# Kernel optimization log

Hardware: AMD Instinct MI355X
Metric: run time of the kernel (lower is better)

The kernel has to match this reference:

```python
import jax, jax.numpy as jnp
import numpy as np

NF = 64        # num_feat
DG = 16        # deformable_groups
K = 3
KK = K * K
CG = NF // DG  # channels per deformable group


def lrelu(x):
    return jnp.where(x >= 0, x, 0.1 * x)


def conv3x3(x, w, b):
    y = jax.lax.conv_general_dilated(
        x, w, window_strides=(1, 1), padding=((1, 1), (1, 1)),
        dimension_numbers=('NCHW', 'OIHW', 'NCHW'))
    return y + b[None, :, None, None]


def _bilinear(feat, py, px):
    # feat: (C, H, W); py, px: arbitrary shape S -> (C,) + S; zeros outside bounds
    H, W = feat.shape[-2:]
    y0f = jnp.floor(py)
    x0f = jnp.floor(px)
    dy = py - y0f
    dx = px - x0f
    y0 = y0f.astype(jnp.int32)
    x0 = x0f.astype(jnp.int32)
    out = jnp.zeros(feat.shape[:1] + py.shape, feat.dtype)
    for yy, xx, wgt in ((y0, x0, (1 - dy) * (1 - dx)),
                        (y0, x0 + 1, (1 - dy) * dx),
                        (y0 + 1, x0, dy * (1 - dx)),
                        (y0 + 1, x0 + 1, dy * dx)):
        valid = (yy >= 0) & (yy < H) & (xx >= 0) & (xx < W)
        v = feat[:, jnp.clip(yy, 0, H - 1), jnp.clip(xx, 0, W - 1)]
        out = out + v * (wgt * valid)[None]
    return out


def backwarp(x, flow):
    # x: (N,C,H,W); flow: (N,2,H,W) with channels (dx, dy) in pixels
    N, C, H, W = x.shape
    gy, gx = jnp.meshgrid(jnp.arange(H, dtype=x.dtype),
                          jnp.arange(W, dtype=x.dtype), indexing='ij')
    px = gx[None] + flow[:, 0]
    py = gy[None] + flow[:, 1]
    return jax.vmap(_bilinear)(x, py, px)


def dcn_v2(x, offset, mask, w, b):
    # x: (N,C,H,W); offset: (N, DG*KK*2, H, W) as consecutive (dy,dx) pairs;
    # mask: (N, DG*KK, H, W) already sigmoided. stride=1, pad=1, k=3.
    N, C, H, W = x.shape
    off = offset.reshape(N, DG, KK, 2, H, W)
    dy, dx = off[:, :, :, 0], off[:, :, :, 1]            # (N,DG,KK,H,W)
    gy, gx = jnp.meshgrid(jnp.arange(H, dtype=x.dtype),
                          jnp.arange(W, dtype=x.dtype), indexing='ij')
    ky = (jnp.arange(KK) // K - K // 2).astype(x.dtype)  # tap row offset: -1,0,1
    kx = (jnp.arange(KK) % K - K // 2).astype(x.dtype)   # tap col offset
    py = dy + gy[None, None, None] + ky[None, None, :, None, None]
    px = dx + gx[None, None, None] + kx[None, None, :, None, None]
    xg = x.reshape(N, DG, CG, H, W)
    sampled = jax.vmap(jax.vmap(_bilinear))(xg, py, px)  # (N,DG,CG,KK,H,W)
    sampled = sampled * mask.reshape(N, DG, 1, KK, H, W)
    wr = w.reshape(-1, DG, CG, KK)                       # (Cout,DG,CG,KK)
    out = jnp.einsum('ngckhw,ogck->nohw', sampled, wr)
    return out + b[None, :, None, None]


def fgda(nbr_feat, ref_feat, flow, w1, b1, w2, b2, w3, b3, w4, b4, dcn_w, dcn_b):
    warped = backwarp(nbr_feat, flow)
    h = lrelu(conv3x3(jnp.concatenate([warped, ref_feat], axis=1), w1, b1))
    h = lrelu(conv3x3(h, w2, b2))
    h = lrelu(conv3x3(h, w3, b3))
    out = conv3x3(h, w4, b4)                             # (N, DG*27, H, W)
    o1, o2, mask = jnp.split(out, 3, axis=1)
    N, _, H, W = flow.shape
    residual = jnp.concatenate([o1, o2], axis=1).reshape(N, -1, 2, H, W)
    # torch.flip(flow, dims=[1]) -> (flow_y, flow_x), broadcast over all taps
    offset = flow[:, ::-1].reshape(N, 1, 2, H, W) + residual
    offset = offset.reshape(N, -1, H, W)
    mask = jax.nn.sigmoid(mask)
    return lrelu(dcn_v2(nbr_feat, offset, mask, dcn_w, dcn_b))


def setup_inputs():
    key = jax.random.key(0)
    ks = jax.random.split(key, 8)
    N, H, W = 8, 128, 128
    s = 0.05
    return {
        'nbr_feat': jax.random.normal(ks[0], (N, NF, H, W), jnp.float32),
        'ref_feat': jax.random.normal(ks[1], (N, NF, H, W), jnp.float32),
        'flow': jax.random.normal(ks[2], (N, 2, H, W), jnp.float32) * 2.0,
        'w1': jax.random.normal(ks[3], (NF, 2 * NF, 3, 3), jnp.float32) * s,
        'b1': jnp.zeros((NF,), jnp.float32),
        'w2': jax.random.normal(ks[4], (NF, NF, 3, 3), jnp.float32) * s,
        'b2': jnp.zeros((NF,), jnp.float32),
        'w3': jax.random.normal(ks[5], (NF, NF, 3, 3), jnp.float32) * s,
        'b3': jnp.zeros((NF,), jnp.float32),
        'w4': jax.random.normal(ks[6], (DG * 3 * KK, NF, 3, 3), jnp.float32) * s,
        'b4': jnp.zeros((DG * 3 * KK,), jnp.float32),
        'dcn_w': jax.random.normal(ks[7], (NF, NF, 3, 3), jnp.float32) * s,
        'dcn_b': jnp.zeros((NF,), jnp.float32),
    }


def reference(nbr_feat, ref_feat, flow, w1, b1, w2, b2, w3, b3, w4, b4, dcn_w, dcn_b):
    return fgda(nbr_feat, ref_feat, flow, w1, b1, w2, b2, w3, b3, w4, b4, dcn_w, dcn_b)
```

## Files before the change

### kernel.cpp

```cpp
#include <hip/hip_runtime.h>
#include <math.h>

#define H 128
#define W 128
#define NB 8
#define NFC 64

typedef __attribute__((ext_vector_type(8))) short s16x8;
typedef __attribute__((ext_vector_type(4))) short s16x4;
typedef __attribute__((ext_vector_type(4))) float f32x4;
typedef __attribute__((ext_vector_type(4))) int   i32x4;
typedef __attribute__((ext_vector_type(2))) int   i32x2;

__device__ __forceinline__ float b2f(short s) {
    return __uint_as_float(((unsigned)(unsigned short)s) << 16);
}
__device__ __forceinline__ short f2bf(float f) {
    unsigned u = __float_as_uint(f);
    u += 0x7FFF + ((u >> 16) & 1);
    return (short)(u >> 16);
}
__device__ __forceinline__ short f2h(float f) {
    _Float16 h = (_Float16)f;
    return __builtin_bit_cast(short, h);
}
__device__ __forceinline__ float h2f(short s) {
    return (float)__builtin_bit_cast(_Float16, s);
}

__global__ __launch_bounds__(256) void k_wt_all(
    const float* __restrict__ w1, const float* __restrict__ w2,
    const float* __restrict__ w3, const float* __restrict__ w4,
    const float* __restrict__ dcw, short* __restrict__ wp)
{
    int idx = blockIdx.x * 256 + threadIdx.x;
    int u = idx / 576;
    int r = idx - u * 576;
    int t = r >> 6, i = r & 63;
    float v;
    if (u < 128) {
        int o = u & 63, icoff = (u >> 6) << 6;
        v = w1[((size_t)(o * 128) + icoff + i) * 9 + t];
    } else if (u < 192) {
        int o = u - 128;
        v = w2[((size_t)(o * 64) + i) * 9 + t];
    } else if (u < 256) {
        int o = u - 192;
        v = w3[((size_t)(o * 64) + i) * 9 + t];
    } else if (u < 704) {
        int o = u - 256;
        v = (o < 432) ? w4[((size_t)(o * 64) + i) * 9 + t] : 0.f;
    } else {
        int o = u - 704;
        v = dcw[((size_t)(o * 64) + i) * 9 + t];
    }
    wp[idx] = f2bf(v);
}

__global__ __launch_bounds__(256) void k_nhwc2(const float* __restrict__ nbr,
                                               const float* __restrict__ ref,
                                               short* __restrict__ nbrG,
                                               short* __restrict__ refH)
{
    int px = blockIdx.x * 256 + threadIdx.x;
    bool isNbr = (px < 131072);
    const float* src;
    if (isNbr) { src = nbr; }
    else       { src = ref; px -= 131072; }
    int n = px >> 14;
    int sp = px & 16383;
    const float* s = src + (size_t)n * 64 * 16384 + sp;
    unsigned pk[32];
    #pragma unroll
    for (int c = 0; c < 32; ++c) {
        float v0 = s[(size_t)(2 * c) * 16384];
        float v1 = s[(size_t)(2 * c + 1) * 16384];
        pk[c] = (unsigned)(unsigned short)f2bf(v0) |
                ((unsigned)(unsigned short)f2bf(v1) << 16);
    }
    if (isNbr) {
        #pragma unroll
        for (int g = 0; g < 16; ++g) {
            i32x2 t;
            t[0] = pk[2 * g]; t[1] = pk[2 * g + 1];
            *(i32x2*)(nbrG + ((size_t)(n * 16 + g) * 16384 + sp) * 4) = t;
        }
    } else {
        i32x4* d = (i32x4*)(refH + (size_t)(n * 16384 + sp) * 64);
        #pragma unroll
        for (int qq = 0; qq < 8; ++qq) {
            i32x4 t;
            t[0] = pk[4 * qq]; t[1] = pk[4 * qq + 1];
            t[2] = pk[4 * qq + 2]; t[3] = pk[4 * qq + 3];
            d[qq] = t;
        }
    }
}

__global__ __launch_bounds__(256) void k_backwarp(const short* __restrict__ nbrG,
                                                  const float* __restrict__ flow,
                                                  short* __restrict__ warped)
{
    int idx = blockIdx.x * 256 + threadIdx.x;
    int px = idx >> 2, qt = idx & 3;
    int n = px >> 14;
    int x = px & 127, y = (px >> 7) & 127;
    float fx = flow[(size_t)(n * 2 + 0) * 16384 + y * 128 + x];
    float fy = flow[(size_t)(n * 2 + 1) * 16384 + y * 128 + x];
    float pxf = (float)x + fx, pyf = (float)y + fy;
    float x0f = floorf(pxf), y0f = floorf(pyf);
    int x0 = (int)x0f, y0 = (int)y0f;
    float dx = pxf - x0f, dy = pyf - y0f;
    float vy0 = ((unsigned)y0 < 128u) ? 1.f : 0.f;
    float vy1 = ((unsigned)(y0 + 1) < 128u) ? 1.f : 0.f;
    float vx0 = ((unsigned)x0 < 128u) ? 1.f : 0.f;
    float vx1 = ((unsigned)(x0 + 1) < 128u) ? 1.f : 0.f;
    float w00 = (1.f - dy) * (1.f - dx) * vy0 * vx0;
    float w01 = (1.f - dy) * dx * vy0 * vx1;
    float w10 = dy * (1.f - dx) * vy1 * vx0;
    float w11 = dy * dx * vy1 * vx1;
    int y0c = min(max(y0, 0), 127), y1c = min(max(y0 + 1, 0), 127);
    int x0c = min(max(x0, 0), 127), x1c = min(max(x0 + 1, 0), 127);
    int xb = min(max(x0, 0), 126);
    bool s0 = (x0c == xb), s1 = (x1c == xb);

    const short* plbase = nbrG + (size_t)n * 16 * 65536;
    s16x8 r0, r1;
    #pragma unroll
    for (int pg = 0; pg < 4; ++pg) {
        const short* pl = plbase + (size_t)(qt * 4 + pg) * 65536;
        s16x8 p0 = *(const s16x8*)(pl + (y0c * 128 + xb) * 4);
        s16x8 p1 = *(const s16x8*)(pl + (y1c * 128 + xb) * 4);
        #pragma unroll
        for (int cc = 0; cc < 4; ++cc) {
            float v00 = b2f(s0 ? p0[cc] : p0[4 + cc]);
            float v01 = b2f(s1 ? p0[cc] : p0[4 + cc]);
            float v10 = b2f(s0 ? p1[cc] : p1[4 + cc]);
            float v11 = b2f(s1 ? p1[cc] : p1[4 + cc]);
            float v = w00 * v00 + w01 * v01 + w10 * v10 + w11 * v11;
            short res = f2bf(v);
            if (pg < 2) r0[pg * 4 + cc] = res;
            else        r1[(pg - 2) * 4 + cc] = res;
        }
    }
    short* o = warped + (size_t)px * 64 + qt * 16;
    *(s16x8*)o = r0;
    *(s16x8*)(o + 8) = r1;
}

template<int MODE>
__global__ __launch_bounds__(256) void k_conv(
    const short* __restrict__ in, const short* __restrict__ wT,
    const float* __restrict__ bias,
    float* __restrict__ partial, short* __restrict__ outB,
    short* __restrict__ offmask, const float* __restrict__ flow, int n0)
{
    __shared__ __align__(16) short tileS[180 * 64];
    __shared__ __align__(16) short aS[64 * 64];

    int tid = threadIdx.x;
    int bid = blockIdx.x;
    int og = (MODE == 3) ? blockIdx.y : 0;
    int n  = (MODE == 3) ? (n0 + (bid >> 7)) : (bid >> 7);
    int tl = bid & 127;
    int bx = (tl & 7) << 4;
    int by = (tl >> 3) << 3;
    int ln = tid & 63, wv = tid >> 6;
    int c = ln & 15, q = ln >> 4;

    for (int i = tid; i < 1440; i += 256) {
        int pt = i >> 3, c16 = i & 7;
        int ty = pt / 18, tx = pt - ty * 18;
        int gy = by + ty - 1, gx = bx + tx - 1;
        i32x4 v = {0, 0, 0, 0};
        if ((unsigned)gy < 128u && (unsigned)gx < 128u)
            v = *(const i32x4*)(in + (((size_t)n * 128 + gy) * 128 + gx) * 64 + c16 * 8);
        *(i32x4*)((char*)tileS + pt * 128 + ((c16 ^ (pt & 7)) << 4)) = v;
    }

    const short* wbase = wT + ((MODE == 3) ? (size_t)og * 36864 : 0);
    int aoc = tid >> 3, ac8 = tid & 7;
    i32x4 sa0 = *(const i32x4*)(wbase + (size_t)aoc * 576 + ac8 * 8);
    i32x4 sa1 = *(const i32x4*)(wbase + (size_t)(aoc + 32) * 576 + ac8 * 8);

    f32x4 acc[4][2];
    #pragma unroll
    for (int m = 0; m < 4; ++m) {
        acc[m][0] = (f32x4){0.f, 0.f, 0.f, 0.f};
        acc[m][1] = (f32x4){0.f, 0.f, 0.f, 0.f};
    }

    int p0 = 2 * wv, p1 = 2 * wv + 1;
    int pby0 = (p0 >> 2) << 2, pbx0 = (p0 & 3) << 2;
    int pby1 = (p1 >> 2) << 2, pbx1 = (p1 & 3) << 2;
    int cy = c >> 2, cx = c & 3;

    __syncthreads();

    for (int tap = 0; tap < 9; ++tap) {
        *(i32x4*)((char*)aS + aoc * 128 + ((ac8 ^ (aoc & 7)) << 4)) = sa0;
        *(i32x4*)((char*)aS + (aoc + 32) * 128 + ((ac8 ^ ((aoc + 32) & 7)) << 4)) = sa1;
        if (tap < 8) {
            sa0 = *(const i32x4*)(wbase + (size_t)aoc * 576 + (tap + 1) * 64 + ac8 * 8);
            sa1 = *(const i32x4*)(wbase + (size_t)(aoc + 32) * 576 + (tap + 1) * 64 + ac8 * 8);
        }
        __syncthreads();

        int dty = tap / 3, dtx = tap - dty * 3;
        int pta = (pby0 + cy + dty) * 18 + pbx0 + cx + dtx;
        int ptb = (pby1 + cy + dty) * 18 + pbx1 + cx + dtx;
        #pragma unroll
        for (int ih = 0; ih < 2; ++ih) {
            int slot = ih * 4 + q;
            s16x8 bf0 = *(const s16x8*)((const char*)tileS + pta * 128 + ((slot ^ (pta & 7)) << 4));
            s16x8 bf1 = *(const s16x8*)((const char*)tileS + ptb * 128 + ((slot ^ (ptb & 7)) << 4));
            #pragma unroll
            for (int m = 0; m < 4; ++m) {
                int ocl = m * 16 + c;
                s16x8 a = *(const s16x8*)((const char*)aS + ocl * 128 + ((slot ^ (ocl & 7)) << 4));
                acc[m][0] = __builtin_amdgcn_mfma_f32_16x16x32_bf16(a, bf0, acc[m][0], 0, 0, 0);
                acc[m][1] = __builtin_amdgcn_mfma_f32_16x16x32_bf16(a, bf1, acc[m][1], 0, 0, 0);
            }
        }
        __syncthreads();
    }

    #pragma unroll
    for (int p = 0; p < 2; ++p) {
        int pby = p ? pby1 : pby0;
        int pbx = p ? pbx1 : pbx0;
        int y = by + pby + cy;
        int x = bx + pbx + cx;
        size_t pxi = ((size_t)n * 128 + y) * 128 + x;
        float fy = 0.f, fx2 = 0.f;
        if (MODE == 3) {
            fy  = flow[(size_t)(n * 2 + 1) * 16384 + y * 128 + x];
            fx2 = flow[(size_t)(n * 2 + 0) * 16384 + y * 128 + x];
        }
        #pragma unroll
        for (int m = 0; m < 4; ++m) {
            int o0 = m * 16 + q * 4;
            f32x4 v = acc[m][p];
            if (MODE == 0) {
                *(f32x4*)(partial + pxi * 64 + o0) = v;
            } else if (MODE == 1 || MODE == 2) {
                f32x4 bv = *(const f32x4*)(bias + o0);
                if (MODE == 1) {
                    f32x4 pv = *(const f32x4*)(partial + pxi * 64 + o0);
                    v += pv;
                }
                v += bv;
                s16x4 r;
                #pragma unroll
                for (int j = 0; j < 4; ++j) {
                    float t = v[j];
                    t = t >= 0.f ? t : 0.1f * t;
                    r[j] = f2bf(t);
                }
                *(s16x4*)(outB + pxi * 64 + o0) = r;
            } else {
                int oc4 = og * 64 + o0;
                if (oc4 < 432) {
                    f32x4 bv = *(const f32x4*)(bias + oc4);
                    v += bv;
                    s16x4 r;
                    if (oc4 < 288) {
                        v[0] += fy; v[1] += fx2; v[2] += fy; v[3] += fx2;
                        #pragma unroll
                        for (int j = 0; j < 4; ++j) r[j] = f2h(v[j]);
                    } else {
                        #pragma unroll
                        for (int j = 0; j < 4; ++j) r[j] = f2h(1.f / (1.f + expf(-v[j])));
                    }
                    size_t nrel = (size_t)(bid >> 7);
                    *(s16x4*)(offmask + (nrel * 16384 + y * 128 + x) * 432 + oc4) = r;
                }
            }
        }
    }
}

__global__ __launch_bounds__(256) void k_dcn(
    const short* __restrict__ offmask, const short* __restrict__ nbrG,
    const short* __restrict__ dcwT, const float* __restrict__ dcb,
    float* __restrict__ out, int n0)
{
    int tid = threadIdx.x;
    int ln = tid & 63, wv = tid >> 6;
    int patch = blockIdx.x * 4 + wv;
    int nrel = patch >> 10;
    int pl = patch & 1023;
    int by = (pl >> 5) << 2, bx = (pl & 31) << 2;
    int n = n0 + nrel;
    int c = ln & 15, q = ln >> 4;
    int y = by + (c >> 2), x = bx + (c & 3);
    const short* om = offmask + ((size_t)nrel * 16384 + y * 128 + x) * 432;
    const short* plbase = nbrG + (size_t)n * 16 * 65536;

    s16x8 bfrag[18];
    #pragma unroll
    for (int tap = 0; tap < 9; ++tap) {
        int dty = tap / 3 - 1, dtx = tap - (tap / 3) * 3 - 1;
        #pragma unroll
        for (int ih = 0; ih < 2; ++ih) {
            s16x8 bf;
            #pragma unroll
            for (int hh = 0; hh < 2; ++hh) {
                int g = ih * 8 + q * 2 + hh;
                int gk = g * 9 + tap;
                int dd = *(const int*)(om + 2 * gk);
                float dyv = h2f((short)(dd & 0xffff));
                float dxv = h2f((short)(dd >> 16));
                float mk  = h2f(om[288 + gk]);
                float sy = (float)(y + dty) + dyv;
                float sx = (float)(x + dtx) + dxv;
                float y0f = floorf(sy), x0f = floorf(sx);
                int y0 = (int)y0f, x0 = (int)x0f;
                float ddy = sy - y0f, ddx = sx - x0f;
                float vy0 = ((unsigned)y0 < 128u) ? 1.f : 0.f;
                float vy1 = ((unsigned)(y0 + 1) < 128u) ? 1.f : 0.f;
                float vx0 = ((unsigned)x0 < 128u) ? 1.f : 0.f;
                float vx1 = ((unsigned)(x0 + 1) < 128u) ? 1.f : 0.f;
                float w00 = (1.f - ddy) * (1.f - ddx) * vy0 * vx0;
                float w01 = (1.f - ddy) * ddx * vy0 * vx1;
                float w10 = ddy * (1.f - ddx) * vy1 * vx0;
                float w11 = ddy * ddx * vy1 * vx1;
                int y0c = min(max(y0, 0), 127), y1c = min(max(y0 + 1, 0), 127);
                int x0c = min(max(x0, 0), 127), x1c = min(max(x0 + 1, 0), 127);
                int xb = min(max(x0, 0), 126);
                bool sel0 = (x0c == xb), sel1 = (x1c == xb);
                const short* plg = plbase + (size_t)g * 65536;
                s16x8 pr0 = *(const s16x8*)(plg + (y0c * 128 + xb) * 4);
                s16x8 pr1 = *(const s16x8*)(plg + (y1c * 128 + xb) * 4);
                #pragma unroll
                for (int cc = 0; cc < 4; ++cc) {
                    float v00 = b2f(sel0 ? pr0[cc] : pr0[4 + cc]);
                    float v01 = b2f(sel1 ? pr0[cc] : pr0[4 + cc]);
                    float v10 = b2f(sel0 ? pr1[cc] : pr1[4 + cc]);
                    float v11 = b2f(sel1 ? pr1[cc] : pr1[4 + cc]);
                    float sv = w00 * v00 + w01 * v01 + w10 * v10 + w11 * v11;
                    bf[hh * 4 + cc] = f2bf(sv * mk);
                }
            }
            bfrag[tap * 2 + ih] = bf;
        }
    }

    f32x4 acc[4];
    #pragma unroll
    for (int m = 0; m < 4; ++m) acc[m] = (f32x4){0.f, 0.f, 0.f, 0.f};
    #pragma unroll
    for (int kc = 0; kc < 18; ++kc) {
        int tap = kc >> 1, ih = kc & 1;
        int ic0 = ih * 32 + q * 8;
        #pragma unroll
        for (int m = 0; m < 4; ++m) {
            s16x8 a = *(const s16x8*)(dcwT + ((size_t)(m * 16 + c) * 9 + tap) * 64 + ic0);
            acc[m] = __builtin_amdgcn_mfma_f32_16x16x32_bf16(a, bfrag[kc], acc[m], 0, 0, 0);
        }
    }
    #pragma unroll
    for (int m = 0; m < 4; ++m) {
        int o0 = m * 16 + q * 4;
        f32x4 bv = *(const f32x4*)(dcb + o0);
        f32x4 v = acc[m] + bv;
        #pragma unroll
        for (int j = 0; j < 4; ++j) {
            float t = v[j];
            t = t >= 0.f ? t : 0.1f * t;
            out[((size_t)n * 64 + o0 + j) * 16384 + y * 128 + x] = t;
        }
    }
}

extern "C" void kernel_launch(void* const* d_in, const int* in_sizes, int n_in,
                              void* d_out, int out_size, void* d_ws, size_t ws_size,
                              hipStream_t stream)
{
    const float* nbr  = (const float*)d_in[0];
    const float* ref  = (const float*)d_in[1];
    const float* flow = (const float*)d_in[2];
    const float* w1   = (const float*)d_in[3];
    const float* b1   = (const float*)d_in[4];
    const float* w2   = (const float*)d_in[5];
    const float* b2   = (const float*)d_in[6];
    const float* w3   = (const float*)d_in[7];
    const float* b3   = (const float*)d_in[8];
    const float* w4   = (const float*)d_in[9];
    const float* b4   = (const float*)d_in[10];
    const float* dcw  = (const float*)d_in[11];
    const float* dcb  = (const float*)d_in[12];
    float* out = (float*)d_out;
    char* ws = (char*)d_ws;

    short* nbrG   = (short*)ws;
    short* wpool  = (short*)(ws + 16777216);
    short* warped = (short*)(ws + 17825792);
    short* refH   = (short*)(ws + 34603008);
    float* h1p    = (float*)(ws + 51380224);
    short* offmask= (short*)(ws + 17825792);
    short* h3     = (short*)(ws + 74448896);
    short* h1     = warped;
    short* h2     = refH;

    short* wT1a = wpool;
    short* wT1b = wpool + 36864;
    short* wT2  = wpool + 73728;
    short* wT3  = wpool + 110592;
    short* wT4  = wpool + 147456;
    short* dcwT = wpool + 405504;

    k_wt_all<<<1728, 256, 0, stream>>>(w1, w2, w3, w4, dcw, wpool);
    k_nhwc2<<<1024, 256, 0, stream>>>(nbr, ref, nbrG, refH);
    k_backwarp<<<2048, 256, 0, stream>>>(nbrG, flow, warped);

    k_conv<0><<<1024, 256, 0, stream>>>(warped, wT1a, nullptr, h1p, nullptr, nullptr, nullptr, 0);
    k_conv<1><<<1024, 256, 0, stream>>>(refH, wT1b, b1, h1p, h1, nullptr, nullptr, 0);
    k_conv<2><<<1024, 256, 0, stream>>>(h1, wT2, b2, nullptr, h2, nullptr, nullptr, 0);
    k_conv<2><<<1024, 256, 0, stream>>>(h2, wT3, b3, nullptr, h3, nullptr, nullptr, 0);

    for (int n0 = 0; n0 < 8; n0 += 4) {
        dim3 g4(512, 7);
        k_conv<3><<<g4, 256, 0, stream>>>(h3, wT4, b4, nullptr, nullptr, offmask, flow, n0);
        k_dcn<<<1024, 256, 0, stream>>>(offmask, nbrG, dcwT, dcb, out, n0);
    }
}
```

Measured before the change: 365.6 us.

## Repack offset/mask per group, interleave DCN sampling with MFMA, rechunk batches

The offset-producing conv now writes offsets and masks into a per-pixel layout padded to 512 halves, with 32 halves per deformable group: 18 offsets followed by 9 masks. The DCN kernel can then load each group's offsets and masks with a few vector loads instead of scattered scalar loads. The DCN kernel also issues MFMAs right after building each tap's B fragment, rather than holding all 18 fragments in registers first, which cuts register pressure and may raise occupancy. The host loop processes batches in chunks of 3 instead of 4, which changes grid sizes and workspace use, and the conv epilogue now does scattered 2-byte and 4-byte stores.

```diff
diff --git a/kernel.cpp b/kernel.cpp
--- a/kernel.cpp
+++ b/kernel.cpp
@@ -263,17 +263,28 @@
                 if (oc4 < 432) {
                     f32x4 bv = *(const f32x4*)(bias + oc4);
                     v += bv;
-                    s16x4 r;
+                    size_t nrel = (size_t)(bid >> 7);
+                    short* pm = offmask + ((size_t)nrel * 16384 + y * 128 + x) * 512;
                     if (oc4 < 288) {
-                        v[0] += fy; v[1] += fx2; v[2] += fy; v[3] += fx2;
+                        int gk0 = oc4 >> 1;
+                        int g0 = gk0 / 9, t0 = gk0 - g0 * 9;
+                        int gk1 = gk0 + 1;
+                        int g1 = gk1 / 9, t1 = gk1 - g1 * 9;
+                        unsigned pk0 = (unsigned)(unsigned short)f2h(v[0] + fy) |
+                                       ((unsigned)(unsigned short)f2h(v[1] + fx2) << 16);
+                        unsigned pk1 = (unsigned)(unsigned short)f2h(v[2] + fy) |
+                                       ((unsigned)(unsigned short)f2h(v[3] + fx2) << 16);
+                        *(int*)(pm + g0 * 32 + t0 * 2) = (int)pk0;
+                        *(int*)(pm + g1 * 32 + t1 * 2) = (int)pk1;
+                    } else {
+                        int gkb = oc4 - 288;
                         #pragma unroll
-                        for (int j = 0; j < 4; ++j) r[j] = f2h(v[j]);
-                    } else {
-                        #pragma unroll
-                        for (int j = 0; j < 4; ++j) r[j] = f2h(1.f / (1.f + expf(-v[j])));
+                        for (int j = 0; j < 4; ++j) {
+                            int gk = gkb + j;
+                            int g = gk / 9, t = gk - g * 9;
+                            pm[g * 32 + 18 + t] = f2h(1.f / (1.f + expf(-v[j])));
+                        }
                     }
-                    size_t nrel = (size_t)(bid >> 7);
-                    *(s16x4*)(offmask + (nrel * 16384 + y * 128 + x) * 432 + oc4) = r;
                 }
             }
         }
@@ -294,24 +305,40 @@
     int n = n0 + nrel;
     int c = ln & 15, q = ln >> 4;
     int y = by + (c >> 2), x = bx + (c & 3);
-    const short* om = offmask + ((size_t)nrel * 16384 + y * 128 + x) * 432;
+    const short* om = offmask + ((size_t)nrel * 16384 + y * 128 + x) * 512;
     const short* plbase = nbrG + (size_t)n * 16 * 65536;
 
-    s16x8 bfrag[18];
-    #pragma unroll
-    for (int tap = 0; tap < 9; ++tap) {
-        int dty = tap / 3 - 1, dtx = tap - (tap / 3) * 3 - 1;
-        #pragma unroll
-        for (int ih = 0; ih < 2; ++ih) {
+    f32x4 acc[4];
+    #pragma unroll
+    for (int m = 0; m < 4; ++m) acc[m] = (f32x4){0.f, 0.f, 0.f, 0.f};
+
+    #pragma unroll
+    for (int ih = 0; ih < 2; ++ih) {
+        int g0 = ih * 8 + q * 2;
+        const short* ob0 = om + g0 * 32;
+        const short* ob1 = om + (g0 + 1) * 32;
+        s16x8 o0[4], o1[4];
+        #pragma unroll
+        for (int k = 0; k < 4; ++k) {
+            o0[k] = *(const s16x8*)(ob0 + k * 8);
+            o1[k] = *(const s16x8*)(ob1 + k * 8);
+        }
+        int ic0 = ih * 32 + q * 8;
+        #pragma unroll
+        for (int tap = 0; tap < 9; ++tap) {
+            int dty = tap / 3 - 1, dtx = tap - (tap / 3) * 3 - 1;
             s16x8 bf;
             #pragma unroll
             for (int hh = 0; hh < 2; ++hh) {
-                int g = ih * 8 + q * 2 + hh;
-                int gk = g * 9 + tap;
-                int dd = *(const int*)(om + 2 * gk);
-                float dyv = h2f((short)(dd & 0xffff));
-                float dxv = h2f((short)(dd >> 16));
-                float mk  = h2f(om[288 + gk]);
+                short sdy = hh ? o1[(2 * tap) >> 3][(2 * tap) & 7]
+                               : o0[(2 * tap) >> 3][(2 * tap) & 7];
+                short sdx = hh ? o1[(2 * tap + 1) >> 3][(2 * tap + 1) & 7]
+                               : o0[(2 * tap + 1) >> 3][(2 * tap + 1) & 7];
+                short smk = hh ? o1[(18 + tap) >> 3][(18 + tap) & 7]
+                               : o0[(18 + tap) >> 3][(18 + tap) & 7];
+                float dyv = h2f(sdy);
+                float dxv = h2f(sdx);
+                float mk  = h2f(smk);
                 float sy = (float)(y + dty) + dyv;
                 float sx = (float)(x + dtx) + dxv;
                 float y0f = floorf(sy), x0f = floorf(sx);
@@ -329,7 +356,7 @@
                 int x0c = min(max(x0, 0), 127), x1c = min(max(x0 + 1, 0), 127);
                 int xb = min(max(x0, 0), 126);
                 bool sel0 = (x0c == xb), sel1 = (x1c == xb);
-                const short* plg = plbase + (size_t)g * 65536;
+                const short* plg = plbase + (size_t)(g0 + hh) * 65536;
                 s16x8 pr0 = *(const s16x8*)(plg + (y0c * 128 + xb) * 4);
                 s16x8 pr1 = *(const s16x8*)(plg + (y1c * 128 + xb) * 4);
                 #pragma unroll
@@ -342,33 +369,24 @@
                     bf[hh * 4 + cc] = f2bf(sv * mk);
                 }
             }
-            bfrag[tap * 2 + ih] = bf;
-        }
-    }
-
-    f32x4 acc[4];
-    #pragma unroll
-    for (int m = 0; m < 4; ++m) acc[m] = (f32x4){0.f, 0.f, 0.f, 0.f};
-    #pragma unroll
-    for (int kc = 0; kc < 18; ++kc) {
-        int tap = kc >> 1, ih = kc & 1;
-        int ic0 = ih * 32 + q * 8;
-        #pragma unroll
-        for (int m = 0; m < 4; ++m) {
-            s16x8 a = *(const s16x8*)(dcwT + ((size_t)(m * 16 + c) * 9 + tap) * 64 + ic0);
-            acc[m] = __builtin_amdgcn_mfma_f32_16x16x32_bf16(a, bfrag[kc], acc[m], 0, 0, 0);
-        }
-    }
+            #pragma unroll
+            for (int m = 0; m < 4; ++m) {
+                s16x8 a = *(const s16x8*)(dcwT + ((size_t)(m * 16 + c) * 9 + tap) * 64 + ic0);
+                acc[m] = __builtin_amdgcn_mfma_f32_16x16x32_bf16(a, bf, acc[m], 0, 0, 0);
+            }
+        }
+    }
+
     #pragma unroll
     for (int m = 0; m < 4; ++m) {
-        int o0 = m * 16 + q * 4;
-        f32x4 bv = *(const f32x4*)(dcb + o0);
+        int o0v = m * 16 + q * 4;
+        f32x4 bv = *(const f32x4*)(dcb + o0v);
         f32x4 v = acc[m] + bv;
         #pragma unroll
         for (int j = 0; j < 4; ++j) {
             float t = v[j];
             t = t >= 0.f ? t : 0.1f * t;
-            out[((size_t)n * 64 + o0 + j) * 16384 + y * 128 + x] = t;
+            out[((size_t)n * 64 + o0v + j) * 16384 + y * 128 + x] = t;
         }
     }
 }
@@ -419,9 +437,11 @@
     k_conv<2><<<1024, 256, 0, stream>>>(h1, wT2, b2, nullptr, h2, nullptr, nullptr, 0);
     k_conv<2><<<1024, 256, 0, stream>>>(h2, wT3, b3, nullptr, h3, nullptr, nullptr, 0);
 
-    for (int n0 = 0; n0 < 8; n0 += 4) {
-        dim3 g4(512, 7);
+    for (int n0 = 0; n0 < 8; ) {
+        int cn = (8 - n0 >= 3) ? 3 : (8 - n0);
+        dim3 g4(cn * 128, 7);
         k_conv<3><<<g4, 256, 0, stream>>>(h3, wT4, b4, nullptr, nullptr, offmask, flow, n0);
-        k_dcn<<<1024, 256, 0, stream>>>(offmask, nbrG, dcwT, dcb, out, n0);
-    }
-}
+        k_dcn<<<cn * 256, 256, 0, stream>>>(offmask, nbrG, dcwT, dcb, out, n0);
+        n0 += cn;
+    }
+}
```

Result: slower. 436.5 us (+19.4%).

## Split DCN taps across two waves per patch with LDS reduction

Applied to the files above, without the earlier changes.

Each 4x4 output patch is now handled by two waves that split the 9 kernel taps (5 and 4), and the partial accumulators are combined through shared memory. The sampling is also interleaved with the MFMAs tap by tap instead of building all 18 B fragments up front, which cuts register pressure. The grid doubles to 2048 blocks to give more parallelism and better latency hiding for the gather loads. The cost is a block-wide barrier, an LDS round trip, and an uneven 5/4 split between the two waves.

```diff
diff --git a/kernel.cpp b/kernel.cpp
--- a/kernel.cpp
+++ b/kernel.cpp
@@ -280,14 +280,73 @@
     }
 }
 
+__device__ __forceinline__ void dcn_tap(
+    int tap, int y, int x, int q, int c,
+    const short* __restrict__ om, const short* __restrict__ plbase,
+    const short* __restrict__ dcwT, f32x4 acc[4])
+{
+    int dty = tap / 3 - 1, dtx = tap - (tap / 3) * 3 - 1;
+    #pragma unroll
+    for (int ih = 0; ih < 2; ++ih) {
+        s16x8 bf;
+        #pragma unroll
+        for (int hh = 0; hh < 2; ++hh) {
+            int g = ih * 8 + q * 2 + hh;
+            int gk = g * 9 + tap;
+            int dd = *(const int*)(om + 2 * gk);
+            float dyv = h2f((short)(dd & 0xffff));
+            float dxv = h2f((short)(dd >> 16));
+            float mk  = h2f(om[288 + gk]);
+            float sy = (float)(y + dty) + dyv;
+            float sx = (float)(x + dtx) + dxv;
+            float y0f = floorf(sy), x0f = floorf(sx);
+            int y0 = (int)y0f, x0 = (int)x0f;
+            float ddy = sy - y0f, ddx = sx - x0f;
+            float vy0 = ((unsigned)y0 < 128u) ? 1.f : 0.f;
+            float vy1 = ((unsigned)(y0 + 1) < 128u) ? 1.f : 0.f;
+            float vx0 = ((unsigned)x0 < 128u) ? 1.f : 0.f;
+            float vx1 = ((unsigned)(x0 + 1) < 128u) ? 1.f : 0.f;
+            float w00 = (1.f - ddy) * (1.f - ddx) * vy0 * vx0;
+            float w01 = (1.f - ddy) * ddx * vy0 * vx1;
+            float w10 = ddy * (1.f - ddx) * vy1 * vx0;
+            float w11 = ddy * ddx * vy1 * vx1;
+            int y0c = min(max(y0, 0), 127), y1c = min(max(y0 + 1, 0), 127);
+            int x0c = min(max(x0, 0), 127), x1c = min(max(x0 + 1, 0), 127);
+            int xb = min(max(x0, 0), 126);
+            bool sel0 = (x0c == xb), sel1 = (x1c == xb);
+            const short* plg = plbase + (size_t)g * 65536;
+            s16x8 pr0 = *(const s16x8*)(plg + (y0c * 128 + xb) * 4);
+            s16x8 pr1 = *(const s16x8*)(plg + (y1c * 128 + xb) * 4);
+            #pragma unroll
+            for (int cc = 0; cc < 4; ++cc) {
+                float v00 = b2f(sel0 ? pr0[cc] : pr0[4 + cc]);
+                float v01 = b2f(sel1 ? pr0[cc] : pr0[4 + cc]);
+                float v10 = b2f(sel0 ? pr1[cc] : pr1[4 + cc]);
+                float v11 = b2f(sel1 ? pr1[cc] : pr1[4 + cc]);
+                float sv = w00 * v00 + w01 * v01 + w10 * v10 + w11 * v11;
+                bf[hh * 4 + cc] = f2bf(sv * mk);
+            }
+        }
+        int ic0 = ih * 32 + q * 8;
+        #pragma unroll
+        for (int m = 0; m < 4; ++m) {
+            s16x8 a = *(const s16x8*)(dcwT + ((size_t)(m * 16 + c) * 9 + tap) * 64 + ic0);
+            acc[m] = __builtin_amdgcn_mfma_f32_16x16x32_bf16(a, bf, acc[m], 0, 0, 0);
+        }
+    }
+}
+
 __global__ __launch_bounds__(256) void k_dcn(
     const short* __restrict__ offmask, const short* __restrict__ nbrG,
     const short* __restrict__ dcwT, const float* __restrict__ dcb,
     float* __restrict__ out, int n0)
 {
+    __shared__ __align__(16) float red[2][64][20];
+
     int tid = threadIdx.x;
     int ln = tid & 63, wv = tid >> 6;
-    int patch = blockIdx.x * 4 + wv;
+    int pll = wv >> 1, khalf = wv & 1;
+    int patch = blockIdx.x * 2 + pll;
     int nrel = patch >> 10;
     int pl = patch & 1023;
     int by = (pl >> 5) << 2, bx = (pl & 31) << 2;
@@ -297,78 +356,41 @@
     const short* om = offmask + ((size_t)nrel * 16384 + y * 128 + x) * 432;
     const short* plbase = nbrG + (size_t)n * 16 * 65536;
 
-    s16x8 bfrag[18];
-    #pragma unroll
-    for (int tap = 0; tap < 9; ++tap) {
-        int dty = tap / 3 - 1, dtx = tap - (tap / 3) * 3 - 1;
-        #pragma unroll
-        for (int ih = 0; ih < 2; ++ih) {
-            s16x8 bf;
+    f32x4 acc[4];
+    #pragma unroll
+    for (int m = 0; m < 4; ++m) acc[m] = (f32x4){0.f, 0.f, 0.f, 0.f};
+
+    if (khalf == 0) {
+        #pragma unroll
+        for (int t = 0; t < 5; ++t) dcn_tap(t, y, x, q, c, om, plbase, dcwT, acc);
+    } else {
+        #pragma unroll
+        for (int t = 5; t < 9; ++t) dcn_tap(t, y, x, q, c, om, plbase, dcwT, acc);
+    }
+
+    if (khalf == 1) {
+        #pragma unroll
+        for (int m = 0; m < 4; ++m)
+            *(f32x4*)&red[pll][ln][m * 4] = acc[m];
+    }
+    __syncthreads();
+    if (khalf == 0) {
+        #pragma unroll
+        for (int m = 0; m < 4; ++m) {
+            f32x4 o = *(const f32x4*)&red[pll][ln][m * 4];
+            acc[m] += o;
+        }
+        #pragma unroll
+        for (int m = 0; m < 4; ++m) {
+            int o0 = m * 16 + q * 4;
+            f32x4 bv = *(const f32x4*)(dcb + o0);
+            f32x4 v = acc[m] + bv;
             #pragma unroll
-            for (int hh = 0; hh < 2; ++hh) {
-                int g = ih * 8 + q * 2 + hh;
-                int gk = g * 9 + tap;
-                int dd = *(const int*)(om + 2 * gk);
-                float dyv = h2f((short)(dd & 0xffff));
-                float dxv = h2f((short)(dd >> 16));
-                float mk  = h2f(om[288 + gk]);
-                float sy = (float)(y + dty) + dyv;
-                float sx = (float)(x + dtx) + dxv;
-                float y0f = floorf(sy), x0f = floorf(sx);
-                int y0 = (int)y0f, x0 = (int)x0f;
-                float ddy = sy - y0f, ddx = sx - x0f;
-                float vy0 = ((unsigned)y0 < 128u) ? 1.f : 0.f;
-                float vy1 = ((unsigned)(y0 + 1) < 128u) ? 1.f : 0.f;
-                float vx0 = ((unsigned)x0 < 128u) ? 1.f : 0.f;
-                float vx1 = ((unsigned)(x0 + 1) < 128u) ? 1.f : 0.f;
-                float w00 = (1.f - ddy) * (1.f - ddx) * vy0 * vx0;
-                float w01 = (1.f - ddy) * ddx * vy0 * vx1;
-                float w10 = ddy * (1.f - ddx) * vy1 * vx0;
-                float w11 = ddy * ddx * vy1 * vx1;
-                int y0c = min(max(y0, 0), 127), y1c = min(max(y0 + 1, 0), 127);
-                int x0c = min(max(x0, 0), 127), x1c = min(max(x0 + 1, 0), 127);
-                int xb = min(max(x0, 0), 126);
-                bool sel0 = (x0c == xb), sel1 = (x1c == xb);
-                const short* plg = plbase + (size_t)g * 65536;
-                s16x8 pr0 = *(const s16x8*)(plg + (y0c * 128 + xb) * 4);
-                s16x8 pr1 = *(const s16x8*)(plg + (y1c * 128 + xb) * 4);
-                #pragma unroll
-                for (int cc = 0; cc < 4; ++cc) {
-                    float v00 = b2f(sel0 ? pr0[cc] : pr0[4 + cc]);
-                    float v01 = b2f(sel1 ? pr0[cc] : pr0[4 + cc]);
-                    float v10 = b2f(sel0 ? pr1[cc] : pr1[4 + cc]);
-                    float v11 = b2f(sel1 ? pr1[cc] : pr1[4 + cc]);
-                    float sv = w00 * v00 + w01 * v01 + w10 * v10 + w11 * v11;
-                    bf[hh * 4 + cc] = f2bf(sv * mk);
-                }
+            for (int j = 0; j < 4; ++j) {
+                float t = v[j];
+                t = t >= 0.f ? t : 0.1f * t;
+                out[((size_t)n * 64 + o0 + j) * 16384 + y * 128 + x] = t;
             }
-            bfrag[tap * 2 + ih] = bf;
-        }
-    }
-
-    f32x4 acc[4];
-    #pragma unroll
-    for (int m = 0; m < 4; ++m) acc[m] = (f32x4){0.f, 0.f, 0.f, 0.f};
-    #pragma unroll
-    for (int kc = 0; kc < 18; ++kc) {
-        int tap = kc >> 1, ih = kc & 1;
-        int ic0 = ih * 32 + q * 8;
-        #pragma unroll
-        for (int m = 0; m < 4; ++m) {
-            s16x8 a = *(const s16x8*)(dcwT + ((size_t)(m * 16 + c) * 9 + tap) * 64 + ic0);
-            acc[m] = __builtin_amdgcn_mfma_f32_16x16x32_bf16(a, bfrag[kc], acc[m], 0, 0, 0);
-        }
-    }
-    #pragma unroll
-    for (int m = 0; m < 4; ++m) {
-        int o0 = m * 16 + q * 4;
-        f32x4 bv = *(const f32x4*)(dcb + o0);
-        f32x4 v = acc[m] + bv;
-        #pragma unroll
-        for (int j = 0; j < 4; ++j) {
-            float t = v[j];
-            t = t >= 0.f ? t : 0.1f * t;
-            out[((size_t)n * 64 + o0 + j) * 16384 + y * 128 + x] = t;
         }
     }
 }
@@ -422,6 +444,6 @@
     for (int n0 = 0; n0 < 8; n0 += 4) {
         dim3 g4(512, 7);
         k_conv<3><<<g4, 256, 0, stream>>>(h3, wT4, b4, nullptr, nullptr, offmask, flow, n0);
-        k_dcn<<<1024, 256, 0, stream>>>(offmask, nbrG, dcwT, dcb, out, n0);
-    }
-}
+        k_dcn<<<2048, 256, 0, stream>>>(offmask, nbrG, dcwT, dcb, out, n0);
+    }
+}
```

Measured after the change: 364.4 us. Within noise of the previous version (-0.3%).
